# Kernel optimization log

Hardware: AMD Instinct MI355X
Metric: run time of the kernel (lower is better)

Reference implementation:

```python
import jax, jax.numpy as jnp
import numpy as np

N = 100000
E = 1600000
D_IN, H1, H2 = 64, 128, 64
ATT = 32


def _mean_aggregate(feat, src, dst, num_nodes):
    # gather source features per edge, scatter-sum to destinations, divide by in-degree
    summed = jax.ops.segment_sum(feat[src], dst, num_segments=num_nodes)  # [N, d]
    deg = jax.ops.segment_sum(jnp.ones((src.shape[0],), feat.dtype), dst, num_segments=num_nodes)
    return summed / jnp.maximum(deg, 1.0)[:, None]


def setup_inputs() -> dict:
    key = jax.random.key(0)
    ks = jax.random.split(key, 16)
    x = jax.random.normal(ks[0], (N, D_IN), dtype=jnp.float32)
    edge_index = jax.random.randint(ks[1], (2, E), 0, N, dtype=jnp.int64)

    def lin(k, fan_in, fan_out):
        bound = 1.0 / np.sqrt(fan_in)
        return jax.random.uniform(k, (fan_in, fan_out), jnp.float32, -bound, bound)

    params = {
        'W1_l': lin(ks[2], D_IN, H1), 'W1_r': lin(ks[3], D_IN, H1),
        'b1': jnp.zeros((H1,), jnp.float32),
        'W2_l': lin(ks[4], H1, H2), 'W2_r': lin(ks[5], H1, H2),
        'b2': jnp.zeros((H2,), jnp.float32),
        'Wa': lin(ks[6], H2, ATT), 'ba': jnp.zeros((ATT,), jnp.float32),
        'ctx': jax.random.normal(ks[7], (ATT,), jnp.float32),
        'Wc1': lin(ks[8], H2, H2 // 2), 'bc1': jnp.zeros((H2 // 2,), jnp.float32),
        'Wc2': lin(ks[9], H2 // 2, 1), 'bc2': jnp.zeros((1,), jnp.float32),
    }
    return {'x': x, 'edge_index': edge_index, **params}


def reference(x, edge_index, W1_l, W1_r, b1, W2_l, W2_r, b2, Wa, ba, ctx, Wc1, bc1, Wc2, bc2):
    src, dst = edge_index[0], edge_index[1]
    ionm_alerts = x[:, -1]  # [N]

    # GraphSAGE layer 1 (mean aggr): lin_l(mean_neighbors) + lin_r(x_self)
    agg1 = _mean_aggregate(x, src, dst, N)
    h = jax.nn.relu(agg1 @ W1_l + b1 + x @ W1_r)  # [N, H1]
    # F.dropout(training=False) -> identity

    # GraphSAGE layer 2
    agg2 = _mean_aggregate(h, src, dst, N)
    h = jax.nn.relu(agg2 @ W2_l + b2 + h @ W2_r)  # [N, H2]

    # attention with IONM alert boost (+0.4)
    scores = jnp.tanh(h @ Wa + ba)            # [N, ATT]
    w = scores @ ctx + ionm_alerts * 0.4       # [N]
    w = jax.nn.softmax(w, axis=0)
    h = h * w[:, None]

    pooled = jnp.mean(h, axis=0, keepdims=True)  # [1, H2]

    # classifier head (Dropout identity in eval)
    z = jax.nn.relu(pooled @ Wc1 + bc1)
    return jax.nn.sigmoid(z @ Wc2 + bc2)  # [1, 1]
```

## Files before the change

kernel.cpp:

```cpp
#include <hip/hip_runtime.h>
#include <math.h>

#define N_NODES 100000
#define E_EDGES 1600000
#define D_IN 64
#define HID1 128
#define HID2 64
#define ATT 32
#define CAP 32
#define AT_STRIDE 136
#define NRANGE 8
#define RNODES (N_NODES / NRANGE)
#define NPART 64
#define XCAST_BLOCKS ((N_NODES * 16 + 255) / 256)
#define NBLK 1024
#define EPB  1563
#define SEGCAP 384
#define SCAT2_BLOCKS 2048
#define GBLK 3125

#define SX 0.4f
#define INVSX 2.5f
#define SV 0.25f
#define INVSV 4.0f

typedef unsigned int uint32;
typedef unsigned short ushort;
typedef __attribute__((ext_vector_type(8))) short short8;
typedef __attribute__((ext_vector_type(4))) float float4v;
typedef __attribute__((ext_vector_type(2))) unsigned int uint32x2;

#define NTL(p) __builtin_nontemporal_load(&(p))

__device__ inline uint32 bf16rn(float f){ uint32 u = __float_as_uint(f); return (u + 0x7fffu + ((u >> 16) & 1u)) >> 16; }
__device__ inline uint32 packbf2(float a, float b){ return bf16rn(a) | (bf16rn(b) << 16); }

__device__ inline int swz3125(int bb){
    int x = bb & 7, k = bb >> 3;
    return (x < 5) ? x * 391 + k : 5 * 391 + (x - 5) * 390 + k;
}

#if __has_builtin(__builtin_amdgcn_cvt_f32_fp8) && __has_builtin(__builtin_amdgcn_cvt_pk_fp8_f32)
#define HW_FP8 1
#endif
#if __has_builtin(__builtin_amdgcn_sdot8)
#define HW_SDOT8 1
#endif

__device__ inline uint32 q4(float v, float inv){
    float n = rintf(v * inv);
    n = fminf(fmaxf(n, -8.f), 7.f);
    return (uint32)((int)n) & 15u;
}

__device__ inline void dec4i(uint32 w, int sh, int& a0, int& a1, int& a2, int& a3){
    a0 += ((int)(w << (28 - sh))) >> 28;
    a1 += ((int)(w << (24 - sh))) >> 28;
    a2 += ((int)(w << (20 - sh))) >> 28;
    a3 += ((int)(w << (16 - sh))) >> 28;
}

__global__ void k_mega(const float* __restrict__ x,
                       const int* __restrict__ src, const int* __restrict__ dst,
                       const float* __restrict__ W1l, const float* __restrict__ W1r,
                       const float* __restrict__ W2l, const float* __restrict__ W2r,
                       uint32* __restrict__ xb, uint32* __restrict__ xq4,
                       uint32* __restrict__ vq4, float* __restrict__ alertv,
                       ushort* __restrict__ wt1g, ushort* __restrict__ wt2g,
                       uint32x2* __restrict__ qu, int* __restrict__ qlen){
    int b = blockIdx.x, t = threadIdx.x;
    if (b < XCAST_BLOCKS){
        int i = b * 256 + t;
        if (i < N_NODES * 16){
            float4v v = NTL(((const float4v*)x)[i]);
            xb[2 * i]     = packbf2(v.x, v.y);
            xb[2 * i + 1] = packbf2(v.z, v.w);
            ((ushort*)xq4)[i] = (ushort)(q4(v.x, INVSX) | (q4(v.y, INVSX) << 4)
                              | (q4(v.z, INVSX) << 8) | (q4(v.w, INVSX) << 12));
            if ((i & 15) == 15) alertv[i >> 4] = v.w;
        }
        return;
    }
    if (b < XCAST_BLOCKS + 2){
        int sub = b - XCAST_BLOCKS;
        ushort* dstp = (sub == 0) ? wt1g : wt2g;
        for (int idx = t; idx < 128 * 128; idx += 256){
            int nn = idx >> 7, kk = idx & 127;
            float v;
            if (sub == 0) v = (kk < 64) ? W1l[kk * 128 + nn] : W1r[(kk - 64) * 128 + nn];
            else          v = (nn < 64) ? W2l[kk * 64 + nn]  : W2r[kk * 64 + (nn - 64)];
            dstp[nn * 128 + kk] = (ushort)bf16rn(v);
        }
        if (sub == 0){
            if (t < 8) xq4[(size_t)N_NODES * 8 + t] = 0u;
            else if (t < 16) vq4[(size_t)N_NODES * 8 + (t - 8)] = 0u;
        }
        return;
    }
    int blk = b - (XCAST_BLOCKS + 2);
    __shared__ int tails[NRANGE];
    if (t < NRANGE) tails[t] = 0;
    __syncthreads();
    int lane = t & 63;
    int base = blk * EPB;
    int end  = min(base + EPB, E_EDGES);
    for (int i0 = base; i0 < end; i0 += 256){
        int i = i0 + t;
        bool v = (i < end);
        int d = 0, s = 0, r = NRANGE;
        if (v){
            d = NTL(dst[i]);
            s = NTL(src[i]);
            r = (int)((uint32)d / (uint32)RNODES);
        }
        int mybase = 0, myoff = 0;
        #pragma unroll
        for (int k = 0; k < NRANGE; k++){
            unsigned long long mk = __ballot(r == k);
            if (r == k){
                int leader = (int)__ffsll((unsigned long long)mk) - 1;
                int nk = (int)__popcll(mk);
                int bse = 0;
                if (lane == leader) bse = atomicAdd(&tails[k], nk);
                bse = __shfl(bse, leader, 64);
                mybase = bse;
                myoff  = (int)__popcll(mk & ((lane == 63) ? 0x7fffffffffffffffull
                                                          : ((1ull << lane) - 1ull)));
            }
        }
        if (v){
            int pos = mybase + myoff;
            if (pos < SEGCAP)
                qu[(size_t)(blk * NRANGE + r) * SEGCAP + pos] = (uint32x2){(uint32)d, (uint32)s};
        }
    }
    __syncthreads();
    if (t < NRANGE) qlen[blk * NRANGE + t] = min(tails[t], SEGCAP);
}

__global__ __launch_bounds__(256) void k_scat2(const uint32x2* __restrict__ qu,
                                               const int* __restrict__ qlen,
                                               int* __restrict__ cnt, int* __restrict__ ssrc){
    int bb = blockIdx.x, t = threadIdx.x;
    int r = bb & (NRANGE - 1);
    int sidx = bb >> 3;
    #pragma unroll 1
    for (int k = 0; k < NBLK / (SCAT2_BLOCKS / NRANGE); k++){
        int seg = sidx * 4 + k;
        int qi = seg * NRANGE + r;
        int len = min(qlen[qi], SEGCAP);
        const uint32x2* qp = &qu[(size_t)qi * SEGCAP];
        for (int i = t; i < len; i += 256){
            uint32x2 pr = NTL(qp[i]);
            int d = (int)pr.x, s = (int)pr.y;
            int pos = atomicAdd(&cnt[d], 1);
            if (pos < CAP) ssrc[d * CAP + pos] = s;
        }
    }
}

__device__ inline void gather8_i4(const uint32* __restrict__ tab4,
                                  const int* __restrict__ ssrc,
                                  const int* __restrict__ cnt,
                                  int n0, int lane,
                                  int acc[8][4], int cct[8]){
    int q = lane >> 4, p = lane & 15;
    int dw = p >> 1, sh = (p & 1) << 4;
#ifdef HW_SDOT8
    uint32 sel0 = 1u << sh;
#endif
    int nn = n0 + (lane & 7);
    int ccl_ = cnt[nn];
    int cc[8];
    #pragma unroll
    for (int j = 0; j < 8; j++){
        int c = __shfl(ccl_, j, 64);
        cct[j] = c;
        cc[j] = min(c, CAP);
    }
    #pragma unroll
    for (int j = 0; j < 8; j++){ acc[j][0] = acc[j][1] = acc[j][2] = acc[j][3] = 0; }
    int cmax = 0;
    #pragma unroll
    for (int j = 0; j < 8; j++) cmax = max(cmax, cc[j]);
    if (cmax == 0) return;
    int se[8];
    #pragma unroll
    for (int j = 0; j < 8; j++)
        se[j] = (lane < cc[j]) ? NTL(ssrc[(n0 + j) * CAP + lane]) : N_NODES;

    uint32 w[4][8];
    #pragma unroll
    for (int g = 0; g < 4; g++){
        #pragma unroll
        for (int j = 0; j < 8; j++){
            int s = __shfl(se[j], g * 4 + q, 64);
            w[g][j] = tab4[(uint32)s * 8u + dw];
        }
    }
    #pragma unroll
    for (int g = 0; g < 4; g++){
        #pragma unroll
        for (int j = 0; j < 8; j++){
#ifdef HW_SDOT8
            acc[j][0] = __builtin_amdgcn_sdot8((int)w[g][j], (int)sel0,         acc[j][0], false);
            acc[j][1] = __builtin_amdgcn_sdot8((int)w[g][j], (int)(sel0 << 4),  acc[j][1], false);
            acc[j][2] = __builtin_amdgcn_sdot8((int)w[g][j], (int)(sel0 << 8),  acc[j][2], false);
            acc[j][3] = __builtin_amdgcn_sdot8((int)w[g][j], (int)(sel0 << 12), acc[j][3], false);
#else
            dec4i(w[g][j], sh, acc[j][0], acc[j][1], acc[j][2], acc[j][3]);
#endif
        }
    }
    if (cmax > 16){
        #pragma unroll
        for (int g = 0; g < 4; g++){
            #pragma unroll
            for (int j = 0; j < 8; j++){
                int s = __shfl(se[j], 16 + g * 4 + q, 64);
                w[g][j] = tab4[(uint32)s * 8u + dw];
            }
        }
        #pragma unroll
        for (int g = 0; g < 4; g++){
            #pragma unroll
            for (int j = 0; j < 8; j++){
#ifdef HW_SDOT8
                acc[j][0] = __builtin_amdgcn_sdot8((int)w[g][j], (int)sel0,         acc[j][0], false);
                acc[j][1] = __builtin_amdgcn_sdot8((int)w[g][j], (int)(sel0 << 4),  acc[j][1], false);
                acc[j][2] = __builtin_amdgcn_sdot8((int)w[g][j], (int)(sel0 << 8),  acc[j][2], false);
                acc[j][3] = __builtin_amdgcn_sdot8((int)w[g][j], (int)(sel0 << 12), acc[j][3], false);
#else
                dec4i(w[g][j], sh, acc[j][0], acc[j][1], acc[j][2], acc[j][3]);
#endif
            }
        }
    }
    #pragma unroll
    for (int j = 0; j < 8; j++){
        acc[j][0] += __shfl_xor(acc[j][0], 16, 64); acc[j][1] += __shfl_xor(acc[j][1], 16, 64);
        acc[j][2] += __shfl_xor(acc[j][2], 16, 64); acc[j][3] += __shfl_xor(acc[j][3], 16, 64);
        acc[j][0] += __shfl_xor(acc[j][0], 32, 64); acc[j][1] += __shfl_xor(acc[j][1], 32, 64);
        acc[j][2] += __shfl_xor(acc[j][2], 32, 64); acc[j][3] += __shfl_xor(acc[j][3], 32, 64);
    }
}

__device__ inline uint32 enc4_unused(){ return 0; }

__device__ inline float inv_deg(int c){ return 1.f / fmaxf(fminf((float)c, (float)CAP), 1.f); }

__global__ __launch_bounds__(256) void k_layer1(
    const uint32* __restrict__ xq4, const uint32* __restrict__ xb,
    const int* __restrict__ ssrc, const int* __restrict__ cnt,
    const ushort* __restrict__ wt1g, const ushort* __restrict__ wt2g,
    const float* __restrict__ b1, const float* __restrict__ b2,
    uint32* __restrict__ vq4, ushort* __restrict__ r2b,
    float* __restrict__ pzero){
    __shared__ ushort smem[2 * 32 * AT_STRIDE];
    ushort* at  = smem;
    ushort* at2 = smem + 32 * AT_STRIDE;
    float* vstage = (float*)smem;
    int t = threadIdx.x, wave = t >> 6, lane = t & 63;
    if (blockIdx.x == 0){
        for (int i = t; i < NPART * 65; i += 256) pzero[i] = 0.f;
    }
    int nb0 = swz3125((int)blockIdx.x) * 32;
    int n0 = nb0 + wave * 8;

    int m0 = t >> 3, ch = t & 7;
    uint4 xval = *(const uint4*)&xb[(size_t)(nb0 + m0) * 32 + ch * 4];

    int acc[8][4]; int cct[8];
    gather8_i4(xq4, ssrc, cnt, n0, lane, acc, cct);
    int p = lane & 15;
    if (lane < 16){
        #pragma unroll
        for (int j = 0; j < 8; j++){
            float f = SX * inv_deg(cct[j]);
            uint2 o;
            o.x = packbf2((float)acc[j][0] * f, (float)acc[j][1] * f);
            o.y = packbf2((float)acc[j][2] * f, (float)acc[j][3] * f);
            *(uint2*)&at[(wave * 8 + j) * AT_STRIDE + 4 * p] = o;
        }
    }
    *(uint4*)((uint32*)(at + m0 * AT_STRIDE + 64) + ch * 4) = xval;
    __syncthreads();

    int cidx = lane & 15, quad = lane >> 4;
    int mt = wave >> 1;
    int nbase = (wave & 1) * 64;
    float4v c[4];
    #pragma unroll
    for (int nt = 0; nt < 4; nt++) c[nt] = (float4v){0.f,0.f,0.f,0.f};
    #pragma unroll
    for (int kt = 0; kt < 4; kt++){
        short8 a = *(short8*)(at + ((mt * 16 + cidx) * AT_STRIDE + kt * 32 + quad * 8));
        #pragma unroll
        for (int nt = 0; nt < 4; nt++){
            short8 b = *(const short8*)(wt1g + ((nbase + nt * 16 + cidx) * 128 + kt * 32 + quad * 8));
            c[nt] = __builtin_amdgcn_mfma_f32_16x16x32_bf16(a, b, c[nt], 0, 0, 0);
        }
    }
    #pragma unroll
    for (int nt = 0; nt < 4; nt++){
        float bb = b1[nbase + nt * 16 + cidx];
        #pragma unroll
        for (int i = 0; i < 4; i++){
            int row = quad * 4 + i;
            at2[(mt * 16 + row) * AT_STRIDE + nbase + nt * 16 + cidx] =
                (ushort)bf16rn(fmaxf(c[nt][i] + bb, 0.f));
        }
    }
    __syncthreads();
    #pragma unroll
    for (int nt = 0; nt < 4; nt++) c[nt] = (float4v){0.f,0.f,0.f,0.f};
    #pragma unroll
    for (int kt = 0; kt < 4; kt++){
        short8 a = *(short8*)(at2 + ((mt * 16 + cidx) * AT_STRIDE + kt * 32 + quad * 8));
        #pragma unroll
        for (int nt = 0; nt < 4; nt++){
            short8 b = *(const short8*)(wt2g + ((nbase + nt * 16 + cidx) * 128 + kt * 32 + quad * 8));
            c[nt] = __builtin_amdgcn_mfma_f32_16x16x32_bf16(a, b, c[nt], 0, 0, 0);
        }
    }
    if (nbase == 0){
        #pragma unroll
        for (int nt = 0; nt < 4; nt++){
            #pragma unroll
            for (int i = 0; i < 4; i++){
                int row = quad * 4 + i;
                vstage[(mt * 16 + row) * 65 + nt * 16 + cidx] = c[nt][i];
            }
        }
    } else {
        #pragma unroll
        for (int nt = 0; nt < 4; nt++){
            float bb = b2[nt * 16 + cidx];
            #pragma unroll
            for (int i = 0; i < 4; i++){
                int row = quad * 4 + i;
                size_t node = nb0 + mt * 16 + row;
                r2b[node * 64 + nt * 16 + cidx] = (ushort)bf16rn(c[nt][i] + bb);
            }
        }
    }
    __syncthreads();
    {
        int m = t >> 3, u = t & 7;
        float f0 = vstage[m * 65 + 8 * u],     f1 = vstage[m * 65 + 8 * u + 1];
        float f2 = vstage[m * 65 + 8 * u + 2], f3 = vstage[m * 65 + 8 * u + 3];
        float f4 = vstage[m * 65 + 8 * u + 4], f5 = vstage[m * 65 + 8 * u + 5];
        float f6 = vstage[m * 65 + 8 * u + 6], f7 = vstage[m * 65 + 8 * u + 7];
        vq4[(size_t)(nb0 + m) * 8 + u] =
              q4(f0, INVSV)        | (q4(f1, INVSV) << 4)  | (q4(f2, INVSV) << 8)
            | (q4(f3, INVSV) << 12)| (q4(f4, INVSV) << 16) | (q4(f5, INVSV) << 20)
            | (q4(f6, INVSV) << 24)| (q4(f7, INVSV) << 28);
    }
}

__device__ inline float bf16lo(uint32 u){ return __uint_as_float(u << 16); }
__device__ inline float bf16hi(uint32 u){ return __uint_as_float(u & 0xffff0000u); }

__global__ __launch_bounds__(256) void k_gather2f(
    const float* __restrict__ alertv, const uint32* __restrict__ vq4,
    const int* __restrict__ ssrc, const int* __restrict__ cnt,
    const ushort* __restrict__ r2b,
    const float* __restrict__ Wa, const float* __restrict__ ba, const float* __restrict__ ctx,
    float* __restrict__ pooledP, float* __restrict__ Zpart){
    __shared__ float sh2[32][68];
    __shared__ float sew[32];
    __shared__ float sp[4][64];
    int t = threadIdx.x, wave = t >> 6, lane = t & 63;
    int bn0 = swz3125((int)blockIdx.x) * 32;
    int n0 = bn0 + wave * 8;
    int acc[8][4]; int cct[8];
    gather8_i4(vq4, ssrc, cnt, n0, lane, acc, cct);
    int p = lane & 15;
    if (lane < 16){
        #pragma unroll
        for (int j = 0; j < 8; j++){
            size_t nj = n0 + j;
            float f = SV * inv_deg(cct[j]);
            uint32x2 rr = NTL(*(const uint32x2*)&r2b[nj * 64 + 4 * p]);
            float4v hv;
            hv.x = fmaxf((float)acc[j][0] * f + bf16lo(rr.x), 0.f);
            hv.y = fmaxf((float)acc[j][1] * f + bf16hi(rr.x), 0.f);
            hv.z = fmaxf((float)acc[j][2] * f + bf16lo(rr.y), 0.f);
            hv.w = fmaxf((float)acc[j][3] * f + bf16hi(rr.y), 0.f);
            *(float4v*)&sh2[wave * 8 + j][4 * p] = hv;
        }
    }
    __syncthreads();
    int node = t >> 3;
    int c0 = (t & 7) * 4;
    float s0 = ba[c0], s1 = ba[c0 + 1], s2 = ba[c0 + 2], s3 = ba[c0 + 3];
    #pragma unroll 8
    for (int j = 0; j < 64; j++){
        float hv = sh2[node][j];
        s0 += hv * Wa[j * ATT + c0];
        s1 += hv * Wa[j * ATT + c0 + 1];
        s2 += hv * Wa[j * ATT + c0 + 2];
        s3 += hv * Wa[j * ATT + c0 + 3];
    }
    float pa = tanhf(s0) * ctx[c0] + tanhf(s1) * ctx[c0 + 1]
             + tanhf(s2) * ctx[c0 + 2] + tanhf(s3) * ctx[c0 + 3];
    #pragma unroll
    for (int off = 4; off >= 1; off >>= 1) pa += __shfl_down(pa, off, 8);
    if ((t & 7) == 0){
        int n = bn0 + node;
        float w = pa + NTL(alertv[n]) * 0.4f;
        sew[node] = expf(w);
    }
    __syncthreads();
    int j = t & 63, q = t >> 6;
    float p4 = 0.f;
    #pragma unroll
    for (int m = 0; m < 8; m++) p4 += sh2[q * 8 + m][j] * sew[q * 8 + m];
    sp[q][j] = p4;
    __syncthreads();
    if (t < 64){
        float s = sp[0][t] + sp[1][t] + sp[2][t] + sp[3][t];
        atomicAdd(&pooledP[(blockIdx.x & (NPART - 1)) * 64 + t], s);
    }
    if (t == 64){
        float z = 0.f;
        #pragma unroll
        for (int m = 0; m < 32; m++) z += sew[m];
        atomicAdd(&Zpart[blockIdx.x & (NPART - 1)], z);
    }
}

__global__ void k_final(const float* __restrict__ pooledP, const float* __restrict__ Zpart,
                        const float* __restrict__ Wc1, const float* __restrict__ bc1,
                        const float* __restrict__ Wc2, const float* __restrict__ bc2,
                        float* __restrict__ out){
    __shared__ float sp[64], sz[32];
    __shared__ float Zs;
    int t = threadIdx.x;
    float s = 0.f;
    for (int q = 0; q < NPART; q++) s += pooledP[q * 64 + t];
    if (t == 0){
        float z = 0.f;
        for (int q = 0; q < NPART; q++) z += Zpart[q];
        Zs = z;
    }
    __syncthreads();
    float scale = 1.0f / (Zs * (float)N_NODES);
    sp[t] = s * scale;
    __syncthreads();
    if (t < 32){
        float a = bc1[t];
        #pragma unroll 8
        for (int j = 0; j < 64; j++) a += sp[j] * Wc1[j * 32 + t];
        sz[t] = fmaxf(a, 0.f);
    }
    __syncthreads();
    if (t == 0){
        float a = bc2[0];
        #pragma unroll
        for (int i = 0; i < 32; i++) a += sz[i] * Wc2[i];
        out[0] = 1.0f / (1.0f + expf(-a));
    }
}

extern "C" void kernel_launch(void* const* d_in, const int* in_sizes, int n_in,
                              void* d_out, int out_size, void* d_ws, size_t ws_size,
                              hipStream_t stream) {
    const float* x   = (const float*)d_in[0];
    const int*   ei  = (const int*)d_in[1];
    const int*   src = ei;
    const int*   dst = ei + E_EDGES;
    const float* W1l = (const float*)d_in[2];
    const float* W1r = (const float*)d_in[3];
    const float* b1  = (const float*)d_in[4];
    const float* W2l = (const float*)d_in[5];
    const float* W2r = (const float*)d_in[6];
    const float* b2  = (const float*)d_in[7];
    const float* Wa  = (const float*)d_in[8];
    const float* ba  = (const float*)d_in[9];
    const float* ctx = (const float*)d_in[10];
    const float* Wc1 = (const float*)d_in[11];
    const float* bc1 = (const float*)d_in[12];
    const float* Wc2 = (const float*)d_in[13];
    const float* bc2 = (const float*)d_in[14];

    char* p = (char*)d_ws;
    int* cnt    = (int*)p;                 p += (size_t)N_NODES * 4;
    int* ssrc   = (int*)p;                 p += (size_t)N_NODES * CAP * 4;
    uint32* xb  = (uint32*)p;              p += (size_t)N_NODES * 32 * 4;
    uint32* xq4 = (uint32*)p;              p += (size_t)(N_NODES + 1) * 8 * 4;
    uint32* vq4 = (uint32*)p;              p += (size_t)(N_NODES + 1) * 8 * 4;
    char* r2region = p;                    p += (size_t)N_NODES * 64 * 4;
    ushort* wt1g = (ushort*)p;             p += 128 * 128 * 2;
    ushort* wt2g = (ushort*)p;             p += 128 * 128 * 2;
    float* pooledP = (float*)p;            p += NPART * 64 * 4;
    float* Zpart   = (float*)p;            p += NPART * 4;
    int* qlen      = (int*)p;              p += (size_t)NBLK * NRANGE * 4;
    float* alertv  = (float*)p;            p += (size_t)N_NODES * 4;
    uint32x2* qu = (uint32x2*)r2region;
    ushort* r2b  = (ushort*)r2region;

    hipMemsetAsync(cnt, 0, (size_t)N_NODES * 4, stream);

    k_mega<<<XCAST_BLOCKS + 2 + NBLK, 256, 0, stream>>>(
        x, src, dst, W1l, W1r, W2l, W2r, xb, xq4, vq4, alertv, wt1g, wt2g, qu, qlen);

    k_scat2<<<SCAT2_BLOCKS, 256, 0, stream>>>(qu, qlen, cnt, ssrc);

    k_layer1<<<GBLK, 256, 0, stream>>>(xq4, xb, ssrc, cnt,
                                       wt1g, wt2g, b1, b2, vq4, r2b, pooledP);
    k_gather2f<<<GBLK, 256, 0, stream>>>(alertv, vq4, ssrc, cnt, r2b,
                                         Wa, ba, ctx, pooledP, Zpart);
    k_final<<<1, 64, 0, stream>>>(pooledP, Zpart, Wc1, bc1, Wc2, bc2, (float*)d_out);
}
```

Measured before the change: 311.6 us.

## Split gather from matmul and attention into separate kernels

Each fused gather+compute kernel becomes two launches. A gather-only kernel writes the bf16 aggregated features to a workspace buffer, and a follow-on kernel (MFMA matmul, or attention) reads them back. The goal is to give the latency-bound gather a lighter kernel with higher occupancy, and to keep the MFMA and attention code from holding registers during the gather. The cost is two extra launches plus a bf16 write and re-read of the aggregate for every node.

```diff
diff --git a/kernel.cpp b/kernel.cpp
--- a/kernel.cpp
+++ b/kernel.cpp
@@ -29,6 +29,7 @@
 typedef __attribute__((ext_vector_type(8))) short short8;
 typedef __attribute__((ext_vector_type(4))) float float4v;
 typedef __attribute__((ext_vector_type(2))) unsigned int uint32x2;
+typedef __attribute__((ext_vector_type(4))) unsigned int uint32x4;
 
 #define NTL(p) __builtin_nontemporal_load(&(p))
 
@@ -40,9 +41,6 @@
     return (x < 5) ? x * 391 + k : 5 * 391 + (x - 5) * 390 + k;
 }
 
-#if __has_builtin(__builtin_amdgcn_cvt_f32_fp8) && __has_builtin(__builtin_amdgcn_cvt_pk_fp8_f32)
-#define HW_FP8 1
-#endif
 #if __has_builtin(__builtin_amdgcn_sdot8)
 #define HW_SDOT8 1
 #endif
@@ -245,44 +243,49 @@
     }
 }
 
-__device__ inline uint32 enc4_unused(){ return 0; }
-
 __device__ inline float inv_deg(int c){ return 1.f / fmaxf(fminf((float)c, (float)CAP), 1.f); }
 
-__global__ __launch_bounds__(256) void k_layer1(
-    const uint32* __restrict__ xq4, const uint32* __restrict__ xb,
+__global__ __launch_bounds__(256) void k_gather(
+    const uint32* __restrict__ tab4,
     const int* __restrict__ ssrc, const int* __restrict__ cnt,
+    float scl, uint32* __restrict__ aggb, float* __restrict__ pzero){
+    int t = threadIdx.x, wave = t >> 6, lane = t & 63;
+    if (pzero != nullptr && blockIdx.x == 0){
+        for (int i = t; i < NPART * 65; i += 256) pzero[i] = 0.f;
+    }
+    int nb0 = swz3125((int)blockIdx.x) * 32;
+    int n0 = nb0 + wave * 8;
+    int acc[8][4]; int cct[8];
+    gather8_i4(tab4, ssrc, cnt, n0, lane, acc, cct);
+    int p = lane & 15;
+    if (lane < 16){
+        #pragma unroll
+        for (int j = 0; j < 8; j++){
+            float f = scl * inv_deg(cct[j]);
+            uint2 o;
+            o.x = packbf2((float)acc[j][0] * f, (float)acc[j][1] * f);
+            o.y = packbf2((float)acc[j][2] * f, (float)acc[j][3] * f);
+            *(uint2*)&aggb[(size_t)(n0 + j) * 32 + 2 * p] = o;
+        }
+    }
+}
+
+__global__ __launch_bounds__(256) void k_mm(
+    const uint32* __restrict__ aggb, const uint32* __restrict__ xb,
     const ushort* __restrict__ wt1g, const ushort* __restrict__ wt2g,
     const float* __restrict__ b1, const float* __restrict__ b2,
-    uint32* __restrict__ vq4, ushort* __restrict__ r2b,
-    float* __restrict__ pzero){
+    uint32* __restrict__ vq4, ushort* __restrict__ r2b){
     __shared__ ushort smem[2 * 32 * AT_STRIDE];
     ushort* at  = smem;
     ushort* at2 = smem + 32 * AT_STRIDE;
     float* vstage = (float*)smem;
     int t = threadIdx.x, wave = t >> 6, lane = t & 63;
-    if (blockIdx.x == 0){
-        for (int i = t; i < NPART * 65; i += 256) pzero[i] = 0.f;
-    }
     int nb0 = swz3125((int)blockIdx.x) * 32;
-    int n0 = nb0 + wave * 8;
 
     int m0 = t >> 3, ch = t & 7;
+    uint4 aval = *(const uint4*)&aggb[(size_t)(nb0 + m0) * 32 + ch * 4];
     uint4 xval = *(const uint4*)&xb[(size_t)(nb0 + m0) * 32 + ch * 4];
-
-    int acc[8][4]; int cct[8];
-    gather8_i4(xq4, ssrc, cnt, n0, lane, acc, cct);
-    int p = lane & 15;
-    if (lane < 16){
-        #pragma unroll
-        for (int j = 0; j < 8; j++){
-            float f = SX * inv_deg(cct[j]);
-            uint2 o;
-            o.x = packbf2((float)acc[j][0] * f, (float)acc[j][1] * f);
-            o.y = packbf2((float)acc[j][2] * f, (float)acc[j][3] * f);
-            *(uint2*)&at[(wave * 8 + j) * AT_STRIDE + 4 * p] = o;
-        }
-    }
+    *(uint4*)((uint32*)(at + m0 * AT_STRIDE) + ch * 4) = aval;
     *(uint4*)((uint32*)(at + m0 * AT_STRIDE + 64) + ch * 4) = xval;
     __syncthreads();
 
@@ -361,34 +364,32 @@
 __device__ inline float bf16lo(uint32 u){ return __uint_as_float(u << 16); }
 __device__ inline float bf16hi(uint32 u){ return __uint_as_float(u & 0xffff0000u); }
 
-__global__ __launch_bounds__(256) void k_gather2f(
-    const float* __restrict__ alertv, const uint32* __restrict__ vq4,
-    const int* __restrict__ ssrc, const int* __restrict__ cnt,
+__global__ __launch_bounds__(256) void k_att(
+    const float* __restrict__ alertv, const uint32* __restrict__ aggvb,
     const ushort* __restrict__ r2b,
     const float* __restrict__ Wa, const float* __restrict__ ba, const float* __restrict__ ctx,
     float* __restrict__ pooledP, float* __restrict__ Zpart){
     __shared__ float sh2[32][68];
     __shared__ float sew[32];
     __shared__ float sp[4][64];
-    int t = threadIdx.x, wave = t >> 6, lane = t & 63;
+    int t = threadIdx.x;
     int bn0 = swz3125((int)blockIdx.x) * 32;
-    int n0 = bn0 + wave * 8;
-    int acc[8][4]; int cct[8];
-    gather8_i4(vq4, ssrc, cnt, n0, lane, acc, cct);
-    int p = lane & 15;
-    if (lane < 16){
-        #pragma unroll
-        for (int j = 0; j < 8; j++){
-            size_t nj = n0 + j;
-            float f = SV * inv_deg(cct[j]);
-            uint32x2 rr = NTL(*(const uint32x2*)&r2b[nj * 64 + 4 * p]);
-            float4v hv;
-            hv.x = fmaxf((float)acc[j][0] * f + bf16lo(rr.x), 0.f);
-            hv.y = fmaxf((float)acc[j][1] * f + bf16hi(rr.x), 0.f);
-            hv.z = fmaxf((float)acc[j][2] * f + bf16lo(rr.y), 0.f);
-            hv.w = fmaxf((float)acc[j][3] * f + bf16hi(rr.y), 0.f);
-            *(float4v*)&sh2[wave * 8 + j][4 * p] = hv;
-        }
+    int m0 = t >> 3, ch = t & 7;
+    {
+        size_t nj = bn0 + m0;
+        uint4 av = *(const uint4*)&aggvb[nj * 32 + ch * 4];
+        uint4 rr = *(const uint4*)&r2b[nj * 64 + ch * 8];
+        float4v h0, h1;
+        h0.x = fmaxf(bf16lo(av.x) + bf16lo(rr.x), 0.f);
+        h0.y = fmaxf(bf16hi(av.x) + bf16hi(rr.x), 0.f);
+        h0.z = fmaxf(bf16lo(av.y) + bf16lo(rr.y), 0.f);
+        h0.w = fmaxf(bf16hi(av.y) + bf16hi(rr.y), 0.f);
+        h1.x = fmaxf(bf16lo(av.z) + bf16lo(rr.z), 0.f);
+        h1.y = fmaxf(bf16hi(av.z) + bf16hi(rr.z), 0.f);
+        h1.z = fmaxf(bf16lo(av.w) + bf16lo(rr.w), 0.f);
+        h1.w = fmaxf(bf16hi(av.w) + bf16hi(rr.w), 0.f);
+        *(float4v*)&sh2[m0][8 * ch]     = h0;
+        *(float4v*)&sh2[m0][8 * ch + 4] = h1;
     }
     __syncthreads();
     int node = t >> 3;
@@ -499,6 +500,7 @@
     float* alertv  = (float*)p;            p += (size_t)N_NODES * 4;
     uint32x2* qu = (uint32x2*)r2region;
     ushort* r2b  = (ushort*)r2region;
+    uint32* aggb = (uint32*)(r2region + (size_t)N_NODES * 128);
 
     hipMemsetAsync(cnt, 0, (size_t)N_NODES * 4, stream);
 
@@ -507,9 +509,9 @@
 
     k_scat2<<<SCAT2_BLOCKS, 256, 0, stream>>>(qu, qlen, cnt, ssrc);
 
-    k_layer1<<<GBLK, 256, 0, stream>>>(xq4, xb, ssrc, cnt,
-                                       wt1g, wt2g, b1, b2, vq4, r2b, pooledP);
-    k_gather2f<<<GBLK, 256, 0, stream>>>(alertv, vq4, ssrc, cnt, r2b,
-                                         Wa, ba, ctx, pooledP, Zpart);
+    k_gather<<<GBLK, 256, 0, stream>>>(xq4, ssrc, cnt, SX, aggb, pooledP);
+    k_mm<<<GBLK, 256, 0, stream>>>(aggb, xb, wt1g, wt2g, b1, b2, vq4, r2b);
+    k_gather<<<GBLK, 256, 0, stream>>>(vq4, ssrc, cnt, SV, aggb, nullptr);
+    k_att<<<GBLK, 256, 0, stream>>>(alertv, aggb, r2b, Wa, ba, ctx, pooledP, Zpart);
     k_final<<<1, 64, 0, stream>>>(pooledP, Zpart, Wc1, bc1, Wc2, bc2, (float*)d_out);
 }
```

Result: slower. 342.2 us (+9.8%).
